# Kernel optimization log

Measured on AMD Instinct MI355X. Metric: run time of the kernel, lower is better.

The kernel has to match this reference:

```python
import jax, jax.numpy as jnp
import numpy as np

B, C, H, W = 2, 256, 64, 64
NH, HD, K = 4, 64, 16  # num_head, head_channel, n_clusters
N = H * W
SCALE = HD ** 0.5


def _lin(x, Wm, b):
    return x @ Wm + b


def _mlp(x, W1, b1, W2, b2):
    h = _lin(x, W1, b1)
    h = jnp.where(h > 0, h, 0.01 * h)  # LeakyReLU(0.01)
    return _lin(h, W2, b2)  # dropout p=0.0 -> identity


def setup_inputs() -> dict:
    key = jax.random.key(0)
    ks = jax.random.split(key, 20)
    s = 1.0 / np.sqrt(C)
    s2 = 1.0 / np.sqrt(2 * C)
    inp = {
        "q_img": jax.random.normal(ks[0], (B, C, H, W), jnp.float32),
        "k_img_map": jax.random.normal(ks[1], (B, C, H, W), jnp.float32),
        "v_img_map": jax.random.normal(ks[2], (B, C, H, W), jnp.float32),
        "labels": jax.random.randint(ks[3], (B, H, W), 0, K),
        "pixel_coefficients": jax.random.uniform(ks[4], (B, N, N), jnp.float32),
        "Wq": jax.random.uniform(ks[5], (C, C), jnp.float32, -s, s),
        "bq": jnp.zeros((C,), jnp.float32),
        "Wk": jax.random.uniform(ks[6], (C, C), jnp.float32, -s, s),
        "bk": jnp.zeros((C,), jnp.float32),
        "Wv": jax.random.uniform(ks[7], (C, C), jnp.float32, -s, s),
        "bv": jnp.zeros((C,), jnp.float32),
        "W11": jax.random.uniform(ks[8], (C, 2 * C), jnp.float32, -s, s),
        "b11": jnp.zeros((2 * C,), jnp.float32),
        "W12": jax.random.uniform(ks[9], (2 * C, C), jnp.float32, -s2, s2),
        "b12": jnp.zeros((C,), jnp.float32),
        "W21": jax.random.uniform(ks[10], (C, 2 * C), jnp.float32, -s, s),
        "b21": jnp.zeros((2 * C,), jnp.float32),
        "W22": jax.random.uniform(ks[11], (2 * C, C), jnp.float32, -s2, s2),
        "b22": jnp.zeros((C,), jnp.float32),
    }
    return inp


def reference(q_img, k_img_map, v_img_map, labels, pixel_coefficients,
              Wq, bq, Wk, bk, Wv, bv, W11, b11, W12, b12, W21, b21, W22, b22):
    # [B,C,H,W] -> [B,N,C]
    q = _lin(q_img.transpose(0, 2, 3, 1).reshape(B, N, C), Wq, bq)
    k = _lin(k_img_map.transpose(0, 2, 3, 1).reshape(B, N, C), Wk, bk)
    v = _lin(v_img_map.transpose(0, 2, 3, 1).reshape(B, N, C), Wv, bv)

    lab = labels.reshape(B, N)
    onehot = (lab[:, :, None] == jnp.arange(K)[None, None, :]).astype(jnp.float32)  # [B,N,K]
    num_k = jnp.einsum('bnk,bnc->bkc', onehot, k)
    den_k = onehot.sum(axis=1)[:, :, None] + 1e-6
    centers_k = num_k / den_k  # [B,K,C]

    qm = q.reshape(B, N, NH, HD).transpose(0, 2, 1, 3)  # [B,h,N,d]
    km = k.reshape(B, N, NH, HD).transpose(0, 2, 1, 3)
    vm = v.reshape(B, N, NH, HD).transpose(0, 2, 1, 3)
    cm = centers_k.reshape(B, K, NH, HD).transpose(0, 2, 1, 3)  # [B,h,K,d]

    attn_intra = jnp.einsum('bhnd,bhmd->bhnm', qm, km)          # [B,h,N,N]
    attn_centers = jnp.einsum('bhnd,bhkd->bhnk', qm, cm)        # [B,h,N,K]

    same = (lab[:, :, None] == lab[:, None, :])[:, None]        # [B,1,N,N]
    idx = jnp.broadcast_to(lab[:, None, None, :], (B, NH, N, N))
    attn_inter = jnp.take_along_axis(attn_centers, idx, axis=-1) * pixel_coefficients[:, None]

    scores = jnp.where(same, attn_intra, attn_inter) / SCALE
    attn = jax.nn.softmax(scores, axis=-1)
    out = jnp.einsum('bhnm,bhmd->bhnd', attn, vm).transpose(0, 2, 1, 3).reshape(B, N, C)

    rs1 = v + _mlp(out, W11, b11, W12, b12)        # [B,N,C] (v_spatial residual)
    rs2 = rs1 + _mlp(rs1, W21, b21, W22, b22)
    return rs2.reshape(B, H, W, C).transpose(0, 3, 1, 2)  # [B,C,H,W]
```

## Files before the change

kernel.cpp:

```cpp
#include <hip/hip_runtime.h>
#include <stdint.h>

#define Bv 2
#define Cv 256
#define Nv 4096
#define NHv 4
#define HDv 64
#define Kv 16


typedef __attribute__((ext_vector_type(8))) short bf16x8;
typedef __attribute__((ext_vector_type(4))) short bf16x4;
typedef __attribute__((ext_vector_type(4))) float f32x4;

__device__ __forceinline__ float bf2f(unsigned short u) {
  union { unsigned int i; float f; } x; x.i = ((unsigned int)u) << 16; return x.f;
}
__device__ __forceinline__ unsigned short f2bf(float f) {
  union { float f; unsigned int i; } x; x.f = f;
  unsigned int r = x.i + 0x7FFF + ((x.i >> 16) & 1);
  return (unsigned short)(r >> 16);
}

__global__ __launch_bounds__(256) void imgt_k(
    const float* __restrict__ qi, const float* __restrict__ ki,
    const float* __restrict__ vi, unsigned short* __restrict__ dst)
{
  const int z = blockIdx.z;
  const float* src = (z < 2 ? qi : (z < 4 ? ki : vi)) + (long long)(z & 1) * Cv * Nv;
  unsigned short* out = dst + (long long)z * Nv * Cv;
  __shared__ float t[32][33];
  const int x = threadIdx.x, y = threadIdx.y;
  const int n0 = blockIdx.x * 32, c0 = blockIdx.y * 32;
  for (int i = y; i < 32; i += 8)
    t[i][x] = src[(long long)(c0 + i) * Nv + n0 + x];
  __syncthreads();
  for (int i = y; i < 32; i += 8)
    out[(long long)(n0 + i) * Cv + c0 + x] = f2bf(t[x][i]);
}

struct WP { const float* p[7]; };

__global__ __launch_bounds__(256) void wt_k(WP wp, unsigned short* __restrict__ dst)
{
  const int z = blockIdx.z;
  const int KD[7] = {256, 256, 256, 256, 512, 256, 512};
  const int ND[7] = {256, 256, 256, 512, 256, 512, 256};
  const long long OFF[7] = {0, 65536, 131072, 196608, 327680, 458752, 589824};
  const int Kw = KD[z], Nw = ND[z];
  const int nb = blockIdx.x * 32, kb2 = blockIdx.y * 32;
  if (nb >= Nw || kb2 >= Kw) return;
  __shared__ float t[32][33];
  const int x = threadIdx.x, y = threadIdx.y;
  const float* src = wp.p[z];
  for (int i = y; i < 32; i += 8)
    t[i][x] = src[(long long)(kb2 + i) * Nw + nb + x];
  __syncthreads();
  for (int i = y; i < 32; i += 8)
    dst[OFF[z] + (long long)(nb + i) * Kw + kb2 + x] = f2bf(t[x][i]);
}

template<bool ABF16, int ACT, int RES, int OM>
__global__ __launch_bounds__(256) void mm_k(
    const void* __restrict__ A, const unsigned short* __restrict__ Bt,
    const float* __restrict__ bias, const float* __restrict__ Res,
    float* __restrict__ outF, unsigned short* __restrict__ outB,
    int M, int Nn, int Kd, long long aBatch, long long oBatch, long long obBatch)
{
  __shared__ __align__(16) unsigned short As[128][72];
  __shared__ __align__(16) unsigned short Bs[128][72];
  const int tid = threadIdx.x;
  const int w = tid >> 6, lane = tid & 63;
  const int lr = lane & 15, quad = lane >> 4;
  const int m0 = blockIdx.x * 128, n0 = blockIdx.y * 128;
  const int z = blockIdx.z;
  const int wm = (w >> 1) * 64, wn = (w & 1) * 64;
  const int sr = tid >> 1, sh = (tid & 1) * 32;

  f32x4 acc[4][4];
#pragma unroll
  for (int i = 0; i < 4; ++i)
#pragma unroll
    for (int j = 0; j < 4; ++j) acc[i][j] = (f32x4){0.f, 0.f, 0.f, 0.f};

  const long long abase = (long long)z * aBatch + (long long)(m0 + sr) * Kd + sh;
  const unsigned short* Bb = Bt + (long long)(n0 + sr) * Kd + sh;

  for (int k0 = 0; k0 < Kd; k0 += 64) {
    if (ABF16) {
      const unsigned short* Ab = (const unsigned short*)A + abase + k0;
      uint4 u0 = *(const uint4*)Ab;
      uint4 u1 = *(const uint4*)(Ab + 8);
      uint4 u2 = *(const uint4*)(Ab + 16);
      uint4 u3 = *(const uint4*)(Ab + 24);
      *(uint4*)&As[sr][sh] = u0;
      *(uint4*)&As[sr][sh + 8] = u1;
      *(uint4*)&As[sr][sh + 16] = u2;
      *(uint4*)&As[sr][sh + 24] = u3;
    } else {
      const float* Af = (const float*)A + abase + k0;
#pragma unroll
      for (int t = 0; t < 4; ++t) {
        const float4 f0 = *(const float4*)(Af + t * 8);
        const float4 f1 = *(const float4*)(Af + t * 8 + 4);
        uint4 pk;
        pk.x = f2bf(f0.x) | ((unsigned int)f2bf(f0.y) << 16);
        pk.y = f2bf(f0.z) | ((unsigned int)f2bf(f0.w) << 16);
        pk.z = f2bf(f1.x) | ((unsigned int)f2bf(f1.y) << 16);
        pk.w = f2bf(f1.z) | ((unsigned int)f2bf(f1.w) << 16);
        *(uint4*)&As[sr][sh + t * 8] = pk;
      }
    }
    {
      const unsigned short* Bp = Bb + k0;
      uint4 u0 = *(const uint4*)Bp;
      uint4 u1 = *(const uint4*)(Bp + 8);
      uint4 u2 = *(const uint4*)(Bp + 16);
      uint4 u3 = *(const uint4*)(Bp + 24);
      *(uint4*)&Bs[sr][sh] = u0;
      *(uint4*)&Bs[sr][sh + 8] = u1;
      *(uint4*)&Bs[sr][sh + 16] = u2;
      *(uint4*)&Bs[sr][sh + 24] = u3;
    }
    __syncthreads();
#pragma unroll
    for (int ks = 0; ks < 2; ++ks) {
      bf16x8 af[4], bfr[4];
#pragma unroll
      for (int i = 0; i < 4; ++i)
        af[i] = *(const bf16x8*)&As[wm + i * 16 + lr][ks * 32 + quad * 8];
#pragma unroll
      for (int j = 0; j < 4; ++j)
        bfr[j] = *(const bf16x8*)&Bs[wn + j * 16 + lr][ks * 32 + quad * 8];
#pragma unroll
      for (int i = 0; i < 4; ++i)
#pragma unroll
        for (int j = 0; j < 4; ++j)
          acc[i][j] = __builtin_amdgcn_mfma_f32_16x16x32_bf16(af[i], bfr[j], acc[i][j], 0, 0, 0);
    }
    __syncthreads();
  }

#pragma unroll
  for (int j = 0; j < 4; ++j) {
    const int col = n0 + wn + j * 16 + lr;
    const float bv = bias[col];
#pragma unroll
    for (int i = 0; i < 4; ++i) {
      const int mb = m0 + wm + i * 16 + quad * 4;
      float r[4];
#pragma unroll
      for (int reg = 0; reg < 4; ++reg) {
        float v = acc[i][j][reg] + bv;
        if (ACT) v = v > 0.f ? v : 0.01f * v;
        if (RES) v += Res[(long long)(mb + reg) * Nn + col];
        r[reg] = v;
      }
      if (OM == 0) {
#pragma unroll
        for (int reg = 0; reg < 4; ++reg)
          outF[(long long)z * oBatch + (long long)(mb + reg) * Nn + col] = r[reg];
      } else if (OM == 1) {
#pragma unroll
        for (int reg = 0; reg < 4; ++reg)
          outB[(long long)z * obBatch + (long long)(mb + reg) * Nn + col] = f2bf(r[reg]);
      } else if (OM == 2) {
#pragma unroll
        for (int reg = 0; reg < 4; ++reg)
          outB[(long long)z * obBatch + (long long)(mb + reg) * Nn + col] = f2bf(r[reg] * 0.125f);
      } else if (OM == 3) {
#pragma unroll
        for (int reg = 0; reg < 4; ++reg)
          outF[(long long)z * oBatch + (long long)(mb + reg) * Nn + col] = r[reg];
        uint2 pk;
        pk.x = f2bf(r[0]) | ((unsigned int)f2bf(r[1]) << 16);
        pk.y = f2bf(r[2]) | ((unsigned int)f2bf(r[3]) << 16);
        *(uint2*)&outB[(long long)z * obBatch + (long long)col * Nv + mb] = pk;
      } else {
        const float4 st = {r[0], r[1], r[2], r[3]};
        *(float4*)&outF[((long long)((mb >> 12) * Cv + col)) * Nv + (mb & 4095)] = st;
      }
    }
  }
}

__global__ __launch_bounds__(256) void zero_k(float* p, int n)
{
  const int i = blockIdx.x * 256 + threadIdx.x;
  if (i < n) p[i] = 0.f;
}

__global__ __launch_bounds__(256) void center_accum(
    const unsigned short* __restrict__ kb, const int* __restrict__ labels,
    float* __restrict__ cent, float* __restrict__ cnts)
{
  const int bx = blockIdx.x;
  const int chunk = bx & 7;
  const int kk = (bx >> 3) & 15;
  const int b = bx >> 7;
  const int c = threadIdx.x;
  const int nbase = chunk * (Nv / 8);
  float acc = 0.f;
  int cnt = 0;
  for (int i = 0; i < Nv / 8; ++i) {
    const int n = nbase + i;
    if (labels[b * Nv + n] == kk) {
      acc += bf2f(kb[(long long)(b * Nv + n) * Cv + c]);
      ++cnt;
    }
  }
  atomicAdd(&cent[(b * Kv + kk) * Cv + c], acc);
  if (c == 0) atomicAdd(&cnts[b * Kv + kk], (float)cnt);
}

__global__ __launch_bounds__(256) void center_norm(float* cent, const float* cnts)
{
  const int i = blockIdx.x * 256 + threadIdx.x;
  cent[i] = cent[i] / (cnts[i >> 8] + 1e-6f);
}

__global__ __launch_bounds__(256) void attn_k(
    const unsigned short* __restrict__ qb, const unsigned short* __restrict__ kb,
    const unsigned short* __restrict__ vtb, const float* __restrict__ cent,
    const int* __restrict__ labels, const float* __restrict__ pc,
    unsigned short* __restrict__ outb)
{
  __shared__ __align__(16) unsigned short q_s[64][72];
  __shared__ __align__(16) unsigned short k_s[64][72];
  __shared__ __align__(16) unsigned short vt_s[64][72];
  __shared__ __align__(16) unsigned short p_s[4][16][68];
  __shared__ float c_s[16][68];
  __shared__ float ac_s[64][17];
  __shared__ int labq_s[64], labm_s[64];

  const int tid = threadIdx.x;
  const int lane = tid & 63, w = tid >> 6;
  const int lr = lane & 15, quad = lane >> 4;
  const int bx = blockIdx.x;
  const int qt = bx & 63, h = (bx >> 6) & 3, b = bx >> 8;
  const int n0 = qt * 64;
  const int sr2 = tid >> 2, so2 = (tid & 3) * 16;

  {
    const unsigned short* src = qb + ((long long)(b * Nv + n0 + sr2)) * Cv + h * HDv + so2;
    *(uint4*)&q_s[sr2][so2] = *(const uint4*)src;
    *(uint4*)&q_s[sr2][so2 + 8] = *(const uint4*)(src + 8);
  }
  if (tid < 64) labq_s[tid] = labels[b * Nv + n0 + tid];
  for (int idx = tid; idx < Kv * HDv; idx += 256)
    c_s[idx >> 6][idx & 63] = cent[((long long)(b * Kv + (idx >> 6))) * Cv + h * HDv + (idx & 63)];
  __syncthreads();
  for (int idx = tid; idx < 64 * Kv; idx += 256) {
    const int r = idx >> 4, kk = idx & 15;
    float s = 0.f;
#pragma unroll
    for (int d = 0; d < HDv; ++d) s += bf2f(q_s[r][d]) * c_s[kk][d];
    ac_s[r][kk] = s;
  }

  const bf16x8 qa0 = *(const bf16x8*)&q_s[w * 16 + lr][quad * 8];
  const bf16x8 qa1 = *(const bf16x8*)&q_s[w * 16 + lr][32 + quad * 8];

  f32x4 oacc[4];
#pragma unroll
  for (int s2 = 0; s2 < 4; ++s2) oacc[s2] = (f32x4){0.f, 0.f, 0.f, 0.f};
  float lrow[4] = {0.f, 0.f, 0.f, 0.f};
  const int row_l = w * 16 + quad * 4;
  const long long pcb = (long long)b * Nv * Nv;

  for (int m0 = 0; m0 < Nv; m0 += 64) {
    __syncthreads();
    {
      const unsigned short* ksrc = kb + ((long long)(b * Nv + m0 + sr2)) * Cv + h * HDv + so2;
      *(uint4*)&k_s[sr2][so2] = *(const uint4*)ksrc;
      *(uint4*)&k_s[sr2][so2 + 8] = *(const uint4*)(ksrc + 8);
      const unsigned short* vsrc = vtb + ((long long)(b * Cv + h * HDv + sr2)) * Nv + m0 + so2;
      *(uint4*)&vt_s[sr2][so2] = *(const uint4*)vsrc;
      *(uint4*)&vt_s[sr2][so2 + 8] = *(const uint4*)(vsrc + 8);
    }
    if (tid < 64) labm_s[tid] = labels[b * Nv + m0 + tid];
    __syncthreads();

    f32x4 sacc[4];
#pragma unroll
    for (int sub = 0; sub < 4; ++sub) {
      const bf16x8 kb0 = *(const bf16x8*)&k_s[sub * 16 + lr][quad * 8];
      const bf16x8 kb1 = *(const bf16x8*)&k_s[sub * 16 + lr][32 + quad * 8];
      f32x4 s = (f32x4){0.f, 0.f, 0.f, 0.f};
      s = __builtin_amdgcn_mfma_f32_16x16x32_bf16(qa0, kb0, s, 0, 0, 0);
      s = __builtin_amdgcn_mfma_f32_16x16x32_bf16(qa1, kb1, s, 0, 0, 0);
      sacc[sub] = s;
    }

    int labm[4];
#pragma unroll
    for (int sub = 0; sub < 4; ++sub) labm[sub] = labm_s[sub * 16 + lr];
    float pcv[4][4], acv[4][4];
#pragma unroll
    for (int sub = 0; sub < 4; ++sub)
#pragma unroll
      for (int reg = 0; reg < 4; ++reg) {
        pcv[sub][reg] = pc[pcb + (long long)(n0 + row_l + reg) * Nv + m0 + sub * 16 + lr];
        acv[sub][reg] = ac_s[row_l + reg][labm[sub]];
      }

#pragma unroll
    for (int reg = 0; reg < 4; ++reg) {
      const int Ln = labq_s[row_l + reg];
#pragma unroll
      for (int sub = 0; sub < 4; ++sub) {
        const float s = (labm[sub] == Ln) ? sacc[sub][reg] : acv[sub][reg] * pcv[sub][reg];
        const float p = __expf(s - 4.0f);
        lrow[reg] += p;
        p_s[w][quad * 4 + reg][sub * 16 + lr] = f2bf(p);
      }
    }

    const bf16x4 p00 = *(const bf16x4*)&p_s[w][lr][quad * 8];
    const bf16x4 p01 = *(const bf16x4*)&p_s[w][lr][quad * 8 + 4];
    const bf16x4 p10 = *(const bf16x4*)&p_s[w][lr][32 + quad * 8];
    const bf16x4 p11 = *(const bf16x4*)&p_s[w][lr][32 + quad * 8 + 4];
    const bf16x8 pa0 = __builtin_shufflevector(p00, p01, 0, 1, 2, 3, 4, 5, 6, 7);
    const bf16x8 pa1 = __builtin_shufflevector(p10, p11, 0, 1, 2, 3, 4, 5, 6, 7);
#pragma unroll
    for (int sub = 0; sub < 4; ++sub) {
      const bf16x8 vb0 = *(const bf16x8*)&vt_s[sub * 16 + lr][quad * 8];
      const bf16x8 vb1 = *(const bf16x8*)&vt_s[sub * 16 + lr][32 + quad * 8];
      oacc[sub] = __builtin_amdgcn_mfma_f32_16x16x32_bf16(pa0, vb0, oacc[sub], 0, 0, 0);
      oacc[sub] = __builtin_amdgcn_mfma_f32_16x16x32_bf16(pa1, vb1, oacc[sub], 0, 0, 0);
    }
  }

#pragma unroll
  for (int reg = 0; reg < 4; ++reg) {
    float l = lrow[reg];
    l += __shfl_xor(l, 1); l += __shfl_xor(l, 2);
    l += __shfl_xor(l, 4); l += __shfl_xor(l, 8);
    const float inv = 1.f / l;
    const long long base = ((long long)(b * Nv + n0 + row_l + reg)) * Cv + h * HDv;
#pragma unroll
    for (int sub = 0; sub < 4; ++sub)
      outb[base + sub * 16 + lr] = f2bf(oacc[sub][reg] * inv);
  }
}

extern "C" void kernel_launch(void* const* d_in, const int* in_sizes, int n_in,
                              void* d_out, int out_size, void* d_ws, size_t ws_size,
                              hipStream_t stream)
{
  const float* q_img = (const float*)d_in[0];
  const float* k_img = (const float*)d_in[1];
  const float* v_img = (const float*)d_in[2];
  const int* labels  = (const int*)d_in[3];
  const float* pc    = (const float*)d_in[4];
  const float* Wq  = (const float*)d_in[5];  const float* bq  = (const float*)d_in[6];
  const float* Wk  = (const float*)d_in[7];  const float* bk  = (const float*)d_in[8];
  const float* Wv  = (const float*)d_in[9];  const float* bv  = (const float*)d_in[10];
  const float* W11 = (const float*)d_in[11]; const float* b11 = (const float*)d_in[12];
  const float* W12 = (const float*)d_in[13]; const float* b12 = (const float*)d_in[14];
  const float* W21 = (const float*)d_in[15]; const float* b21 = (const float*)d_in[16];
  const float* W22 = (const float*)d_in[17]; const float* b22 = (const float*)d_in[18];
  float* outp = (float*)d_out;

  const long long SZ = (long long)Bv * Nv * Cv;
  float* ws   = (float*)d_ws;
  float* vpp  = ws;
  float* rs1  = vpp + SZ;
  float* cent = rs1 + SZ;
  float* cnts = cent + Bv * Kv * Cv;
  unsigned short* wt   = (unsigned short*)(cnts + Bv * Kv);
  unsigned short* qbf  = wt + 720896;
  unsigned short* kbf  = qbf + SZ;
  unsigned short* vtb  = kbf + SZ;
  unsigned short* aob  = vtb + SZ;
  unsigned short* h1b  = aob + SZ;
  unsigned short* imgT = aob;

  const long long NvCv = (long long)Nv * Cv;

  imgt_k<<<dim3(Nv / 32, Cv / 32, 6), dim3(32, 8), 0, stream>>>(q_img, k_img, v_img, imgT);
  WP wp = {{Wq, Wk, Wv, W11, W12, W21, W22}};
  wt_k<<<dim3(16, 16, 7), dim3(32, 8), 0, stream>>>(wp, wt);

  mm_k<true, 0, 0, 2><<<dim3(32, 2, 2), 256, 0, stream>>>(
      imgT, wt, bq, nullptr, nullptr, qbf, Nv, Cv, Cv, NvCv, 0, NvCv);
  mm_k<true, 0, 0, 1><<<dim3(32, 2, 2), 256, 0, stream>>>(
      imgT + 2 * NvCv, wt + 65536, bk, nullptr, nullptr, kbf, Nv, Cv, Cv, NvCv, 0, NvCv);
  mm_k<true, 0, 0, 3><<<dim3(32, 2, 2), 256, 0, stream>>>(
      imgT + 4 * NvCv, wt + 131072, bv, nullptr, vpp, vtb, Nv, Cv, Cv, NvCv, NvCv, NvCv);

  zero_k<<<dim3(33), 256, 0, stream>>>(cent, Bv * Kv * Cv + Bv * Kv);
  center_accum<<<dim3(Bv * Kv * 8), 256, 0, stream>>>(kbf, labels, cent, cnts);
  center_norm<<<dim3(Bv * Kv * Cv / 256), 256, 0, stream>>>(cent, cnts);

  attn_k<<<dim3(64 * NHv * Bv), 256, 0, stream>>>(qbf, kbf, vtb, cent, labels, pc, aob);

  mm_k<true, 1, 0, 1><<<dim3(64, 4, 1), 256, 0, stream>>>(
      aob, wt + 196608, b11, nullptr, nullptr, h1b, 2 * Nv, 2 * Cv, Cv, 0, 0, 0);
  mm_k<true, 0, 1, 0><<<dim3(64, 2, 1), 256, 0, stream>>>(
      h1b, wt + 327680, b12, vpp, rs1, nullptr, 2 * Nv, Cv, 2 * Cv, 0, 0, 0);

  mm_k<false, 1, 0, 1><<<dim3(64, 4, 1), 256, 0, stream>>>(
      rs1, wt + 458752, b21, nullptr, nullptr, h1b, 2 * Nv, 2 * Cv, Cv, 0, 0, 0);
  mm_k<true, 0, 1, 4><<<dim3(64, 2, 1), 256, 0, stream>>>(
      h1b, wt + 589824, b22, rs1, outp, nullptr, 2 * Nv, Cv, 2 * Cv, 0, 0, 0);
}
```

Measured before the change: 482.5 us.

## Split attention keys across two partitions, prefetch tiles, fuse QKV projections

The attention kernel now splits the key dimension into two halves, doubling the grid to 1024 blocks. Each half writes unnormalized fp32 partial outputs and row sums, and a new combine kernel merges them into bf16. K/V tiles, labels and pixel coefficients for the next step are prefetched into registers while the current tile computes. The three QKV projection launches are merged into one kernel, and center accumulation stages labels in shared memory. The split adds extra fp32 partial buffers and another pass over them, and the register prefetch raises register pressure.

```diff
diff --git a/kernel.cpp b/kernel.cpp
--- a/kernel.cpp
+++ b/kernel.cpp
@@ -10,7 +10,6 @@
 
 
 typedef __attribute__((ext_vector_type(8))) short bf16x8;
-typedef __attribute__((ext_vector_type(4))) short bf16x4;
 typedef __attribute__((ext_vector_type(4))) float f32x4;
 
 __device__ __forceinline__ float bf2f(unsigned short u) {
@@ -60,12 +59,11 @@
     dst[OFF[z] + (long long)(nb + i) * Kw + kb2 + x] = f2bf(t[x][i]);
 }
 
-template<bool ABF16, int ACT, int RES, int OM>
-__global__ __launch_bounds__(256) void mm_k(
-    const void* __restrict__ A, const unsigned short* __restrict__ Bt,
-    const float* __restrict__ bias, const float* __restrict__ Res,
-    float* __restrict__ outF, unsigned short* __restrict__ outB,
-    int M, int Nn, int Kd, long long aBatch, long long oBatch, long long obBatch)
+__global__ __launch_bounds__(256) void proj_k(
+    const unsigned short* __restrict__ imgT, const unsigned short* __restrict__ wt,
+    const float* __restrict__ bq, const float* __restrict__ bk, const float* __restrict__ bv,
+    unsigned short* __restrict__ qbf, unsigned short* __restrict__ kbf,
+    float* __restrict__ vpp, unsigned short* __restrict__ vtb)
 {
   __shared__ __align__(16) unsigned short As[128][72];
   __shared__ __align__(16) unsigned short Bs[128][72];
@@ -73,9 +71,14 @@
   const int w = tid >> 6, lane = tid & 63;
   const int lr = lane & 15, quad = lane >> 4;
   const int m0 = blockIdx.x * 128, n0 = blockIdx.y * 128;
-  const int z = blockIdx.z;
+  const int z = blockIdx.z, zz = z >> 1, bb = z & 1;
   const int wm = (w >> 1) * 64, wn = (w & 1) * 64;
   const int sr = tid >> 1, sh = (tid & 1) * 32;
+  const long long NvCv = (long long)Nv * Cv;
+
+  const float* bias = zz == 0 ? bq : (zz == 1 ? bk : bv);
+  const unsigned short* Ab0 = imgT + (long long)z * NvCv + (long long)(m0 + sr) * Cv + sh;
+  const unsigned short* Bb0 = wt + (long long)zz * 65536 + (long long)(n0 + sr) * Cv + sh;
 
   f32x4 acc[4][4];
 #pragma unroll
@@ -83,20 +86,100 @@
 #pragma unroll
     for (int j = 0; j < 4; ++j) acc[i][j] = (f32x4){0.f, 0.f, 0.f, 0.f};
 
-  const long long abase = (long long)z * aBatch + (long long)(m0 + sr) * Kd + sh;
+  for (int k0 = 0; k0 < Cv; k0 += 64) {
+    const unsigned short* Ab = Ab0 + k0;
+    const unsigned short* Bp = Bb0 + k0;
+    uint4 a0 = *(const uint4*)Ab, a1 = *(const uint4*)(Ab + 8);
+    uint4 a2 = *(const uint4*)(Ab + 16), a3 = *(const uint4*)(Ab + 24);
+    uint4 b0 = *(const uint4*)Bp, b1 = *(const uint4*)(Bp + 8);
+    uint4 b2 = *(const uint4*)(Bp + 16), b3 = *(const uint4*)(Bp + 24);
+    *(uint4*)&As[sr][sh] = a0; *(uint4*)&As[sr][sh + 8] = a1;
+    *(uint4*)&As[sr][sh + 16] = a2; *(uint4*)&As[sr][sh + 24] = a3;
+    *(uint4*)&Bs[sr][sh] = b0; *(uint4*)&Bs[sr][sh + 8] = b1;
+    *(uint4*)&Bs[sr][sh + 16] = b2; *(uint4*)&Bs[sr][sh + 24] = b3;
+    __syncthreads();
+#pragma unroll
+    for (int ks = 0; ks < 2; ++ks) {
+      bf16x8 af[4], bfr[4];
+#pragma unroll
+      for (int i = 0; i < 4; ++i)
+        af[i] = *(const bf16x8*)&As[wm + i * 16 + lr][ks * 32 + quad * 8];
+#pragma unroll
+      for (int j = 0; j < 4; ++j)
+        bfr[j] = *(const bf16x8*)&Bs[wn + j * 16 + lr][ks * 32 + quad * 8];
+#pragma unroll
+      for (int i = 0; i < 4; ++i)
+#pragma unroll
+        for (int j = 0; j < 4; ++j)
+          acc[i][j] = __builtin_amdgcn_mfma_f32_16x16x32_bf16(af[i], bfr[j], acc[i][j], 0, 0, 0);
+    }
+    __syncthreads();
+  }
+
+#pragma unroll
+  for (int j = 0; j < 4; ++j) {
+    const int col = n0 + wn + j * 16 + lr;
+    const float bvv = bias[col];
+#pragma unroll
+    for (int i = 0; i < 4; ++i) {
+      const int mb = m0 + wm + i * 16 + quad * 4;
+      float r[4];
+#pragma unroll
+      for (int reg = 0; reg < 4; ++reg) r[reg] = acc[i][j][reg] + bvv;
+      const long long ob = (long long)bb * NvCv;
+      if (zz == 0) {
+#pragma unroll
+        for (int reg = 0; reg < 4; ++reg)
+          qbf[ob + (long long)(mb + reg) * Cv + col] = f2bf(r[reg] * 0.125f);
+      } else if (zz == 1) {
+#pragma unroll
+        for (int reg = 0; reg < 4; ++reg)
+          kbf[ob + (long long)(mb + reg) * Cv + col] = f2bf(r[reg]);
+      } else {
+#pragma unroll
+        for (int reg = 0; reg < 4; ++reg)
+          vpp[ob + (long long)(mb + reg) * Cv + col] = r[reg];
+        uint2 pk;
+        pk.x = f2bf(r[0]) | ((unsigned int)f2bf(r[1]) << 16);
+        pk.y = f2bf(r[2]) | ((unsigned int)f2bf(r[3]) << 16);
+        *(uint2*)&vtb[ob + (long long)col * Nv + mb] = pk;
+      }
+    }
+  }
+}
+
+template<bool ABF16, int ACT, int RES, int OM>
+__global__ __launch_bounds__(256) void mm_k(
+    const void* __restrict__ A, const unsigned short* __restrict__ Bt,
+    const float* __restrict__ bias, const float* __restrict__ Res,
+    float* __restrict__ outF, unsigned short* __restrict__ outB,
+    int M, int Nn, int Kd)
+{
+  __shared__ __align__(16) unsigned short As[128][72];
+  __shared__ __align__(16) unsigned short Bs[128][72];
+  const int tid = threadIdx.x;
+  const int w = tid >> 6, lane = tid & 63;
+  const int lr = lane & 15, quad = lane >> 4;
+  const int m0 = blockIdx.x * 128, n0 = blockIdx.y * 128;
+  const int wm = (w >> 1) * 64, wn = (w & 1) * 64;
+  const int sr = tid >> 1, sh = (tid & 1) * 32;
+
+  f32x4 acc[4][4];
+#pragma unroll
+  for (int i = 0; i < 4; ++i)
+#pragma unroll
+    for (int j = 0; j < 4; ++j) acc[i][j] = (f32x4){0.f, 0.f, 0.f, 0.f};
+
+  const long long abase = (long long)(m0 + sr) * Kd + sh;
   const unsigned short* Bb = Bt + (long long)(n0 + sr) * Kd + sh;
 
   for (int k0 = 0; k0 < Kd; k0 += 64) {
     if (ABF16) {
       const unsigned short* Ab = (const unsigned short*)A + abase + k0;
-      uint4 u0 = *(const uint4*)Ab;
-      uint4 u1 = *(const uint4*)(Ab + 8);
-      uint4 u2 = *(const uint4*)(Ab + 16);
-      uint4 u3 = *(const uint4*)(Ab + 24);
-      *(uint4*)&As[sr][sh] = u0;
-      *(uint4*)&As[sr][sh + 8] = u1;
-      *(uint4*)&As[sr][sh + 16] = u2;
-      *(uint4*)&As[sr][sh + 24] = u3;
+      uint4 u0 = *(const uint4*)Ab, u1 = *(const uint4*)(Ab + 8);
+      uint4 u2 = *(const uint4*)(Ab + 16), u3 = *(const uint4*)(Ab + 24);
+      *(uint4*)&As[sr][sh] = u0; *(uint4*)&As[sr][sh + 8] = u1;
+      *(uint4*)&As[sr][sh + 16] = u2; *(uint4*)&As[sr][sh + 24] = u3;
     } else {
       const float* Af = (const float*)A + abase + k0;
 #pragma unroll
@@ -113,14 +196,10 @@
     }
     {
       const unsigned short* Bp = Bb + k0;
-      uint4 u0 = *(const uint4*)Bp;
-      uint4 u1 = *(const uint4*)(Bp + 8);
-      uint4 u2 = *(const uint4*)(Bp + 16);
-      uint4 u3 = *(const uint4*)(Bp + 24);
-      *(uint4*)&Bs[sr][sh] = u0;
-      *(uint4*)&Bs[sr][sh + 8] = u1;
-      *(uint4*)&Bs[sr][sh + 16] = u2;
-      *(uint4*)&Bs[sr][sh + 24] = u3;
+      uint4 u0 = *(const uint4*)Bp, u1 = *(const uint4*)(Bp + 8);
+      uint4 u2 = *(const uint4*)(Bp + 16), u3 = *(const uint4*)(Bp + 24);
+      *(uint4*)&Bs[sr][sh] = u0; *(uint4*)&Bs[sr][sh + 8] = u1;
+      *(uint4*)&Bs[sr][sh + 16] = u2; *(uint4*)&Bs[sr][sh + 24] = u3;
     }
     __syncthreads();
 #pragma unroll
@@ -159,23 +238,11 @@
       if (OM == 0) {
 #pragma unroll
         for (int reg = 0; reg < 4; ++reg)
-          outF[(long long)z * oBatch + (long long)(mb + reg) * Nn + col] = r[reg];
+          outF[(long long)(mb + reg) * Nn + col] = r[reg];
       } else if (OM == 1) {
 #pragma unroll
         for (int reg = 0; reg < 4; ++reg)
-          outB[(long long)z * obBatch + (long long)(mb + reg) * Nn + col] = f2bf(r[reg]);
-      } else if (OM == 2) {
-#pragma unroll
-        for (int reg = 0; reg < 4; ++reg)
-          outB[(long long)z * obBatch + (long long)(mb + reg) * Nn + col] = f2bf(r[reg] * 0.125f);
-      } else if (OM == 3) {
-#pragma unroll
-        for (int reg = 0; reg < 4; ++reg)
-          outF[(long long)z * oBatch + (long long)(mb + reg) * Nn + col] = r[reg];
-        uint2 pk;
-        pk.x = f2bf(r[0]) | ((unsigned int)f2bf(r[1]) << 16);
-        pk.y = f2bf(r[2]) | ((unsigned int)f2bf(r[3]) << 16);
-        *(uint2*)&outB[(long long)z * obBatch + (long long)col * Nv + mb] = pk;
+          outB[(long long)(mb + reg) * Nn + col] = f2bf(r[reg]);
       } else {
         const float4 st = {r[0], r[1], r[2], r[3]};
         *(float4*)&outF[((long long)((mb >> 12) * Cv + col)) * Nv + (mb & 4095)] = st;
@@ -194,18 +261,21 @@
     const unsigned short* __restrict__ kb, const int* __restrict__ labels,
     float* __restrict__ cent, float* __restrict__ cnts)
 {
+  __shared__ int lab_s[512];
   const int bx = blockIdx.x;
   const int chunk = bx & 7;
   const int kk = (bx >> 3) & 15;
   const int b = bx >> 7;
   const int c = threadIdx.x;
-  const int nbase = chunk * (Nv / 8);
+  const int nbase = chunk * 512;
+  for (int i = threadIdx.x; i < 512; i += 256) lab_s[i] = labels[b * Nv + nbase + i];
+  __syncthreads();
   float acc = 0.f;
   int cnt = 0;
-  for (int i = 0; i < Nv / 8; ++i) {
-    const int n = nbase + i;
-    if (labels[b * Nv + n] == kk) {
-      acc += bf2f(kb[(long long)(b * Nv + n) * Cv + c]);
+#pragma unroll 4
+  for (int i = 0; i < 512; ++i) {
+    if (lab_s[i] == kk) {
+      acc += bf2f(kb[(long long)(b * Nv + nbase + i) * Cv + c]);
       ++cnt;
     }
   }
@@ -218,68 +288,94 @@
   const int i = blockIdx.x * 256 + threadIdx.x;
   cent[i] = cent[i] / (cnts[i >> 8] + 1e-6f);
 }
+
+union PSCS {
+  unsigned short p[4][16][68];
+  float c[16][68];
+};
 
 __global__ __launch_bounds__(256) void attn_k(
     const unsigned short* __restrict__ qb, const unsigned short* __restrict__ kb,
     const unsigned short* __restrict__ vtb, const float* __restrict__ cent,
     const int* __restrict__ labels, const float* __restrict__ pc,
-    unsigned short* __restrict__ outb)
+    float* __restrict__ opart, float* __restrict__ lpart)
 {
   __shared__ __align__(16) unsigned short q_s[64][72];
   __shared__ __align__(16) unsigned short k_s[64][72];
   __shared__ __align__(16) unsigned short vt_s[64][72];
-  __shared__ __align__(16) unsigned short p_s[4][16][68];
-  __shared__ float c_s[16][68];
+  __shared__ __align__(16) PSCS u_s;
   __shared__ float ac_s[64][17];
-  __shared__ int labq_s[64], labm_s[64];
 
   const int tid = threadIdx.x;
   const int lane = tid & 63, w = tid >> 6;
   const int lr = lane & 15, quad = lane >> 4;
   const int bx = blockIdx.x;
-  const int qt = bx & 63, h = (bx >> 6) & 3, b = bx >> 8;
+  const int qt = bx & 63, h = (bx >> 6) & 3, b = (bx >> 8) & 1;
+  const int part = bx >> 9;
   const int n0 = qt * 64;
+  const int mbase = part * 2048;
   const int sr2 = tid >> 2, so2 = (tid & 3) * 16;
+  const int row_l = w * 16 + quad * 4;
+  const long long pcb = (long long)b * Nv * Nv;
 
   {
     const unsigned short* src = qb + ((long long)(b * Nv + n0 + sr2)) * Cv + h * HDv + so2;
     *(uint4*)&q_s[sr2][so2] = *(const uint4*)src;
     *(uint4*)&q_s[sr2][so2 + 8] = *(const uint4*)(src + 8);
   }
-  if (tid < 64) labq_s[tid] = labels[b * Nv + n0 + tid];
   for (int idx = tid; idx < Kv * HDv; idx += 256)
-    c_s[idx >> 6][idx & 63] = cent[((long long)(b * Kv + (idx >> 6))) * Cv + h * HDv + (idx & 63)];
+    u_s.c[idx >> 6][idx & 63] = cent[((long long)(b * Kv + (idx >> 6))) * Cv + h * HDv + (idx & 63)];
+
+  uint4 ka0, ka1, va0, va1;
+  float pc1[4][4];
+  int labm1[4], labq[4];
+  {
+    const long long ks = ((long long)(b * Nv + mbase + sr2)) * Cv + h * HDv + so2;
+    ka0 = *(const uint4*)(kb + ks); ka1 = *(const uint4*)(kb + ks + 8);
+    const long long vs = ((long long)(b * Cv + h * HDv + sr2)) * Nv + mbase + so2;
+    va0 = *(const uint4*)(vtb + vs); va1 = *(const uint4*)(vtb + vs + 8);
+  }
+#pragma unroll
+  for (int sub = 0; sub < 4; ++sub) {
+    labm1[sub] = labels[b * Nv + mbase + sub * 16 + lr];
+#pragma unroll
+    for (int reg = 0; reg < 4; ++reg)
+      pc1[sub][reg] = pc[pcb + (long long)(n0 + row_l + reg) * Nv + mbase + sub * 16 + lr];
+  }
+#pragma unroll
+  for (int reg = 0; reg < 4; ++reg) labq[reg] = labels[b * Nv + n0 + row_l + reg];
+
   __syncthreads();
   for (int idx = tid; idx < 64 * Kv; idx += 256) {
     const int r = idx >> 4, kk = idx & 15;
     float s = 0.f;
 #pragma unroll
-    for (int d = 0; d < HDv; ++d) s += bf2f(q_s[r][d]) * c_s[kk][d];
+    for (int d = 0; d < HDv; ++d) s += bf2f(q_s[r][d]) * u_s.c[kk][d];
     ac_s[r][kk] = s;
   }
-
   const bf16x8 qa0 = *(const bf16x8*)&q_s[w * 16 + lr][quad * 8];
   const bf16x8 qa1 = *(const bf16x8*)&q_s[w * 16 + lr][32 + quad * 8];
+  __syncthreads();
+
+  *(uint4*)&k_s[sr2][so2] = ka0; *(uint4*)&k_s[sr2][so2 + 8] = ka1;
+  *(uint4*)&vt_s[sr2][so2] = va0; *(uint4*)&vt_s[sr2][so2 + 8] = va1;
+  __syncthreads();
 
   f32x4 oacc[4];
 #pragma unroll
   for (int s2 = 0; s2 < 4; ++s2) oacc[s2] = (f32x4){0.f, 0.f, 0.f, 0.f};
   float lrow[4] = {0.f, 0.f, 0.f, 0.f};
-  const int row_l = w * 16 + quad * 4;
-  const long long pcb = (long long)b * Nv * Nv;
-
-  for (int m0 = 0; m0 < Nv; m0 += 64) {
-    __syncthreads();
-    {
-      const unsigned short* ksrc = kb + ((long long)(b * Nv + m0 + sr2)) * Cv + h * HDv + so2;
-      *(uint4*)&k_s[sr2][so2] = *(const uint4*)ksrc;
-      *(uint4*)&k_s[sr2][so2 + 8] = *(const uint4*)(ksrc + 8);
-      const unsigned short* vsrc = vtb + ((long long)(b * Cv + h * HDv + sr2)) * Nv + m0 + so2;
-      *(uint4*)&vt_s[sr2][so2] = *(const uint4*)vsrc;
-      *(uint4*)&vt_s[sr2][so2 + 8] = *(const uint4*)(vsrc + 8);
-    }
-    if (tid < 64) labm_s[tid] = labels[b * Nv + m0 + tid];
-    __syncthreads();
+
+  for (int t = 0; t < 32; ++t) {
+    const int m0 = mbase + t * 64;
+    const bool has = (t < 31);
+
+    if (has) {
+      const long long ks = ((long long)(b * Nv + m0 + 64 + sr2)) * Cv + h * HDv + so2;
+      ka0 = *(const uint4*)(kb + ks); ka1 = *(const uint4*)(kb + ks + 8);
+      const long long vs = ((long long)(b * Cv + h * HDv + sr2)) * Nv + m0 + 64 + so2;
+      va0 = *(const uint4*)(vtb + vs); va1 = *(const uint4*)(vtb + vs + 8);
+    }
 
     f32x4 sacc[4];
 #pragma unroll
@@ -292,36 +388,31 @@
       sacc[sub] = s;
     }
 
-    int labm[4];
-#pragma unroll
-    for (int sub = 0; sub < 4; ++sub) labm[sub] = labm_s[sub * 16 + lr];
-    float pcv[4][4], acv[4][4];
-#pragma unroll
-    for (int sub = 0; sub < 4; ++sub)
-#pragma unroll
-      for (int reg = 0; reg < 4; ++reg) {
-        pcv[sub][reg] = pc[pcb + (long long)(n0 + row_l + reg) * Nv + m0 + sub * 16 + lr];
-        acv[sub][reg] = ac_s[row_l + reg][labm[sub]];
-      }
-
 #pragma unroll
     for (int reg = 0; reg < 4; ++reg) {
-      const int Ln = labq_s[row_l + reg];
+      const int Ln = labq[reg];
 #pragma unroll
       for (int sub = 0; sub < 4; ++sub) {
-        const float s = (labm[sub] == Ln) ? sacc[sub][reg] : acv[sub][reg] * pcv[sub][reg];
+        const float s = (labm1[sub] == Ln) ? sacc[sub][reg]
+                                           : ac_s[row_l + reg][labm1[sub]] * pc1[sub][reg];
         const float p = __expf(s - 4.0f);
         lrow[reg] += p;
-        p_s[w][quad * 4 + reg][sub * 16 + lr] = f2bf(p);
+        u_s.p[w][quad * 4 + reg][sub * 16 + lr] = f2bf(p);
       }
     }
 
-    const bf16x4 p00 = *(const bf16x4*)&p_s[w][lr][quad * 8];
-    const bf16x4 p01 = *(const bf16x4*)&p_s[w][lr][quad * 8 + 4];
-    const bf16x4 p10 = *(const bf16x4*)&p_s[w][lr][32 + quad * 8];
-    const bf16x4 p11 = *(const bf16x4*)&p_s[w][lr][32 + quad * 8 + 4];
-    const bf16x8 pa0 = __builtin_shufflevector(p00, p01, 0, 1, 2, 3, 4, 5, 6, 7);
-    const bf16x8 pa1 = __builtin_shufflevector(p10, p11, 0, 1, 2, 3, 4, 5, 6, 7);
+    if (has) {
+#pragma unroll
+      for (int sub = 0; sub < 4; ++sub) {
+        labm1[sub] = labels[b * Nv + m0 + 64 + sub * 16 + lr];
+#pragma unroll
+        for (int reg = 0; reg < 4; ++reg)
+          pc1[sub][reg] = pc[pcb + (long long)(n0 + row_l + reg) * Nv + m0 + 64 + sub * 16 + lr];
+      }
+    }
+
+    const bf16x8 pa0 = *(const bf16x8*)&u_s.p[w][lr][quad * 8];
+    const bf16x8 pa1 = *(const bf16x8*)&u_s.p[w][lr][32 + quad * 8];
 #pragma unroll
     for (int sub = 0; sub < 4; ++sub) {
       const bf16x8 vb0 = *(const bf16x8*)&vt_s[sub * 16 + lr][quad * 8];
@@ -329,6 +420,13 @@
       oacc[sub] = __builtin_amdgcn_mfma_f32_16x16x32_bf16(pa0, vb0, oacc[sub], 0, 0, 0);
       oacc[sub] = __builtin_amdgcn_mfma_f32_16x16x32_bf16(pa1, vb1, oacc[sub], 0, 0, 0);
     }
+
+    __syncthreads();
+    if (has) {
+      *(uint4*)&k_s[sr2][so2] = ka0; *(uint4*)&k_s[sr2][so2 + 8] = ka1;
+      *(uint4*)&vt_s[sr2][so2] = va0; *(uint4*)&vt_s[sr2][so2 + 8] = va1;
+    }
+    __syncthreads();
   }
 
 #pragma unroll
@@ -336,12 +434,31 @@
     float l = lrow[reg];
     l += __shfl_xor(l, 1); l += __shfl_xor(l, 2);
     l += __shfl_xor(l, 4); l += __shfl_xor(l, 8);
-    const float inv = 1.f / l;
-    const long long base = ((long long)(b * Nv + n0 + row_l + reg)) * Cv + h * HDv;
+    const int row = n0 + row_l + reg;
+    const long long obase = (long long)part * 2097152 + ((long long)(b * Nv + row)) * Cv + h * HDv;
 #pragma unroll
     for (int sub = 0; sub < 4; ++sub)
-      outb[base + sub * 16 + lr] = f2bf(oacc[sub][reg] * inv);
-  }
+      opart[obase + sub * 16 + lr] = oacc[sub][reg];
+    if (lr == 0)
+      lpart[part * 32768 + (b * 4 + h) * 4096 + row] = l;
+  }
+}
+
+__global__ __launch_bounds__(256) void combine_k(
+    const float* __restrict__ op, const float* __restrict__ lp,
+    unsigned short* __restrict__ aob)
+{
+  const long long i4 = ((long long)blockIdx.x * 256 + threadIdx.x) * 4;
+  const int c = (int)(i4 & 255), n = (int)((i4 >> 8) & 4095), b = (int)(i4 >> 20);
+  const int h = c >> 6;
+  const float l = lp[(b * 4 + h) * 4096 + n] + lp[32768 + (b * 4 + h) * 4096 + n];
+  const float inv = 1.f / l;
+  const float4 a = *(const float4*)&op[i4];
+  const float4 d = *(const float4*)&op[2097152 + i4];
+  uint2 pk;
+  pk.x = f2bf((a.x + d.x) * inv) | ((unsigned int)f2bf((a.y + d.y) * inv) << 16);
+  pk.y = f2bf((a.z + d.z) * inv) | ((unsigned int)f2bf((a.w + d.w) * inv) << 16);
+  *(uint2*)&aob[i4] = pk;
 }
 
 extern "C" void kernel_launch(void* const* d_in, const int* in_sizes, int n_in,
@@ -363,11 +480,13 @@
   float* outp = (float*)d_out;
 
   const long long SZ = (long long)Bv * Nv * Cv;
-  float* ws   = (float*)d_ws;
-  float* vpp  = ws;
-  float* rs1  = vpp + SZ;
-  float* cent = rs1 + SZ;
-  float* cnts = cent + Bv * Kv * Cv;
+  float* ws    = (float*)d_ws;
+  float* vpp   = ws;
+  float* rs1   = vpp + SZ;
+  float* opart = rs1 + SZ;
+  float* lpart = opart + 2 * SZ;
+  float* cent  = lpart + 65536;
+  float* cnts  = cent + Bv * Kv * Cv;
   unsigned short* wt   = (unsigned short*)(cnts + Bv * Kv);
   unsigned short* qbf  = wt + 720896;
   unsigned short* kbf  = qbf + SZ;
@@ -376,32 +495,26 @@
   unsigned short* h1b  = aob + SZ;
   unsigned short* imgT = aob;
 
-  const long long NvCv = (long long)Nv * Cv;
-
   imgt_k<<<dim3(Nv / 32, Cv / 32, 6), dim3(32, 8), 0, stream>>>(q_img, k_img, v_img, imgT);
   WP wp = {{Wq, Wk, Wv, W11, W12, W21, W22}};
   wt_k<<<dim3(16, 16, 7), dim3(32, 8), 0, stream>>>(wp, wt);
 
-  mm_k<true, 0, 0, 2><<<dim3(32, 2, 2), 256, 0, stream>>>(
-      imgT, wt, bq, nullptr, nullptr, qbf, Nv, Cv, Cv, NvCv, 0, NvCv);
-  mm_k<true, 0, 0, 1><<<dim3(32, 2, 2), 256, 0, stream>>>(
-      imgT + 2 * NvCv, wt + 65536, bk, nullptr, nullptr, kbf, Nv, Cv, Cv, NvCv, 0, NvCv);
-  mm_k<true, 0, 0, 3><<<dim3(32, 2, 2), 256, 0, stream>>>(
-      imgT + 4 * NvCv, wt + 131072, bv, nullptr, vpp, vtb, Nv, Cv, Cv, NvCv, NvCv, NvCv);
+  proj_k<<<dim3(32, 2, 6), 256, 0, stream>>>(imgT, wt, bq, bk, bv, qbf, kbf, vpp, vtb);
 
   zero_k<<<dim3(33), 256, 0, stream>>>(cent, Bv * Kv * Cv + Bv * Kv);
   center_accum<<<dim3(Bv * Kv * 8), 256, 0, stream>>>(kbf, labels, cent, cnts);
   center_norm<<<dim3(Bv * Kv * Cv / 256), 256, 0, stream>>>(cent, cnts);
 
-  attn_k<<<dim3(64 * NHv * Bv), 256, 0, stream>>>(qbf, kbf, vtb, cent, labels, pc, aob);
-
-  mm_k<true, 1, 0, 1><<<dim3(64, 4, 1), 256, 0, stream>>>(
-      aob, wt + 196608, b11, nullptr, nullptr, h1b, 2 * Nv, 2 * Cv, Cv, 0, 0, 0);
-  mm_k<true, 0, 1, 0><<<dim3(64, 2, 1), 256, 0, stream>>>(
-      h1b, wt + 327680, b12, vpp, rs1, nullptr, 2 * Nv, Cv, 2 * Cv, 0, 0, 0);
-
-  mm_k<false, 1, 0, 1><<<dim3(64, 4, 1), 256, 0, stream>>>(
-      rs1, wt + 458752, b21, nullptr, nullptr, h1b, 2 * Nv, 2 * Cv, Cv, 0, 0, 0);
-  mm_k<true, 0, 1, 4><<<dim3(64, 2, 1), 256, 0, stream>>>(
-      h1b, wt + 589824, b22, rs1, outp, nullptr, 2 * Nv, Cv, 2 * Cv, 0, 0, 0);
-}
+  attn_k<<<dim3(1024), 256, 0, stream>>>(qbf, kbf, vtb, cent, labels, pc, opart, lpart);
+  combine_k<<<dim3(2048), 256, 0, stream>>>(opart, lpart, aob);
+
+  mm_k<true, 1, 0, 1><<<dim3(64, 4), 256, 0, stream>>>(
+      aob, wt + 196608, b11, nullptr, nullptr, h1b, 2 * Nv, 2 * Cv, Cv);
+  mm_k<true, 0, 1, 0><<<dim3(64, 2), 256, 0, stream>>>(
+      h1b, wt + 327680, b12, vpp, rs1, nullptr, 2 * Nv, Cv, 2 * Cv);
+
+  mm_k<false, 1, 0, 1><<<dim3(64, 4), 256, 0, stream>>>(
+      rs1, wt + 458752, b21, nullptr, nullptr, h1b, 2 * Nv, 2 * Cv, Cv);
+  mm_k<true, 0, 1, 4><<<dim3(64, 2), 256, 0, stream>>>(
+      h1b, wt + 589824, b22, rs1, outp, nullptr, 2 * Nv, Cv, 2 * Cv);
+}
```

Result: faster. 450.3 us (-6.7%).
